# Performance work log

Measured on AMD Instinct MI355X. Metric: run time of the kernel, lower is better.

## Reference

```python
import jax, jax.numpy as jnp
import numpy as np
from jax import lax

IMG_DIM = 512
D_MODEL = 768
N_LAYER = 12
D_INNER = 2 * D_MODEL          # 1536
D_STATE = 16
D_CONV = 4
DT_RANK = (D_MODEL + 15) // 16 # 48
BATCH = 4
SEQ = 256


def setup_inputs() -> dict:
    key = jax.random.key(0)
    ks = jax.random.split(key, 16)
    s = 0.02
    inp = {
        "frames_rep": jax.random.normal(ks[0], (BATCH, SEQ, IMG_DIM), jnp.float32),
        "fproj_w": jax.random.normal(ks[1], (IMG_DIM, D_MODEL), jnp.float32) * s,
        "fproj_b": jnp.zeros((D_MODEL,), jnp.float32),
        "norm_w": jnp.ones((N_LAYER, D_MODEL), jnp.float32),
        "in_w": jax.random.normal(ks[2], (N_LAYER, D_MODEL, 2 * D_INNER), jnp.float32) * s,
        "conv_w": jax.random.normal(ks[3], (N_LAYER, D_INNER, D_CONV), jnp.float32) * s,
        "conv_b": jnp.zeros((N_LAYER, D_INNER), jnp.float32),
        "xproj_w": jax.random.normal(ks[4], (N_LAYER, D_INNER, DT_RANK + 2 * D_STATE), jnp.float32) * s,
        "dt_w": jax.random.normal(ks[5], (N_LAYER, DT_RANK, D_INNER), jnp.float32) * s,
        "dt_b": jnp.full((N_LAYER, D_INNER), -2.0, jnp.float32),  # softplus(-2)~0.13
        "A_log": jnp.broadcast_to(jnp.log(jnp.arange(1, D_STATE + 1, dtype=jnp.float32)), (N_LAYER, D_INNER, D_STATE)) * jnp.ones((N_LAYER, D_INNER, 1)),
        "D_param": jnp.ones((N_LAYER, D_INNER), jnp.float32),
        "out_w": jax.random.normal(ks[6], (N_LAYER, D_INNER, D_MODEL), jnp.float32) * s,
        "normf_w": jnp.ones((D_MODEL,), jnp.float32),
    }
    return inp


def _rmsnorm(x, w, eps=1e-5):
    return x * lax.rsqrt(jnp.mean(x * x, axis=-1, keepdims=True) + eps) * w


def _mamba_layer(x, in_w, conv_w, conv_b, xproj_w, dt_w, dt_b, A_log, D_param, out_w):
    # x: (B, L, D_MODEL)
    B, L, _ = x.shape
    xz = x @ in_w                                  # (B, L, 2*di)
    xi, res = jnp.split(xz, 2, axis=-1)            # each (B, L, di)
    # depthwise causal conv over time
    xc = jnp.transpose(xi, (0, 2, 1))              # (B, di, L)
    xc = lax.conv_general_dilated(
        xc, conv_w[:, None, :], (1,), [(D_CONV - 1, 0)],
        feature_group_count=D_INNER)
    xi = jax.nn.silu(jnp.transpose(xc + conv_b[None, :, None], (0, 2, 1)))
    # input-dependent SSM parameters
    x_dbl = xi @ xproj_w                           # (B, L, dt_rank + 2n)
    delta = x_dbl[..., :DT_RANK]
    Bm = x_dbl[..., DT_RANK:DT_RANK + D_STATE]     # (B, L, n)
    Cm = x_dbl[..., DT_RANK + D_STATE:]            # (B, L, n)
    delta = jax.nn.softplus(delta @ dt_w + dt_b)   # (B, L, di)
    A = -jnp.exp(A_log)                            # (di, n)
    deltaA = jnp.exp(delta[..., None] * A)                               # (B, L, di, n)
    deltaBu = delta[..., None] * Bm[:, :, None, :] * xi[..., None]       # (B, L, di, n)

    def step(h, inp):
        dA, dBu, c = inp
        h = dA * h + dBu                           # (B, di, n)
        y = jnp.einsum('bdn,bn->bd', h, c)
        return h, y

    xs = (deltaA.transpose(1, 0, 2, 3), deltaBu.transpose(1, 0, 2, 3), Cm.transpose(1, 0, 2))
    h0 = jnp.zeros((B, D_INNER, D_STATE), x.dtype)
    _, ys = lax.scan(step, h0, xs)                 # (L, B, di)
    y = ys.transpose(1, 0, 2) + xi * D_param
    y = y * jax.nn.silu(res)
    return y @ out_w                               # (B, L, D_MODEL)


def reference(frames_rep, fproj_w, fproj_b, norm_w, in_w, conv_w, conv_b,
              xproj_w, dt_w, dt_b, A_log, D_param, out_w, normf_w):
    h = jax.nn.relu(frames_rep @ fproj_w + fproj_b)       # (B, L, D_MODEL)
    for i in range(N_LAYER):
        h = h + _mamba_layer(_rmsnorm(h, norm_w[i]), in_w[i], conv_w[i], conv_b[i],
                             xproj_w[i], dt_w[i], dt_b[i], A_log[i], D_param[i], out_w[i])
    return _rmsnorm(h, normf_w)
```

## Files before the change

### kernel.cpp

```cpp
#include <hip/hip_runtime.h>
#include <hip/hip_bf16.h>
#include <cmath>

#define IMG_DIM 512
#define D_MODEL 768
#define N_LAYER 12
#define D_INNER 1536
#define D_STATE 16
#define D_CONV 4
#define DT_RANK 48
#define BATCH 4
#define SEQ 256
#define M_TOK (BATCH * SEQ)
#define XPROJ_N (DT_RANK + 2 * D_STATE)
#define KSPLIT 16
#define NCHUNK 16
#define CLEN 16
#define LOG2E 1.4426950408889634f

typedef __attribute__((ext_vector_type(8))) short bf16x8;
typedef __attribute__((ext_vector_type(8))) unsigned short u16x8;
typedef __attribute__((ext_vector_type(4))) float f32x4;
typedef __hip_bfloat16 bf16;

__device__ __forceinline__ float softplus_f(float v) {
    return v > 20.f ? v : log1pf(expf(v));
}
__device__ __forceinline__ float b2f(bf16 v) { return __bfloat162float(v); }
__device__ __forceinline__ float us2f(unsigned short v) {
    return __uint_as_float(((unsigned)v) << 16);
}

__device__ __forceinline__ void gl_lds16(const char* g, char* l) {
    __builtin_amdgcn_global_load_lds(
        (const __attribute__((address_space(1))) unsigned int*)g,
        (__attribute__((address_space(3))) unsigned int*)l,
        16, 0, 0);
}

__global__ __launch_bounds__(256) void wcvt_t_k(
    const float* __restrict__ W, bf16* __restrict__ WT, int K, int N)
{
    __shared__ float tile[32][33];
    W  += (size_t)blockIdx.z * K * N;
    WT += (size_t)blockIdx.z * K * N;
    const int tx = threadIdx.x & 31;
    const int ty4 = (threadIdx.x >> 5) * 4;
    const int n0 = blockIdx.x * 32, k0 = blockIdx.y * 32;
    #pragma unroll
    for (int r = 0; r < 4; ++r)
        tile[ty4 + r][tx] = (n0 + tx < N)
            ? W[(size_t)(k0 + ty4 + r) * N + n0 + tx] : 0.f;
    __syncthreads();
    #pragma unroll
    for (int r = 0; r < 4; ++r)
        if (n0 + ty4 + r < N)
            WT[(size_t)(n0 + ty4 + r) * K + k0 + tx] =
                __float2bfloat16(tile[tx][ty4 + r]);
}

__global__ __launch_bounds__(256) void cvt_bf16_k(
    const float* __restrict__ in, bf16* __restrict__ out, int n)
{
    int i = blockIdx.x * 256 + threadIdx.x;
    if (i < n) out[i] = __float2bfloat16(in[i]);
}

__global__ __launch_bounds__(256) void dtw_cvt_k(
    const float* __restrict__ dt_w, bf16* __restrict__ dtwT)
{
    int idx = blockIdx.x * 256 + threadIdx.x;
    int k = idx & 63;
    int n = (idx >> 6) % D_INNER;
    int l = idx / (64 * D_INNER);
    dtwT[idx] = (k < DT_RANK)
        ? __float2bfloat16(dt_w[((size_t)l * DT_RANK + k) * D_INNER + n])
        : bf16(0.f);
}

__global__ __launch_bounds__(256) void a2_k(
    const float* __restrict__ A_log, float* __restrict__ A2)
{
    int idx = blockIdx.x * 256 + threadIdx.x;
    A2[idx] = -expf(A_log[idx]) * LOG2E;
}

template <int EPI, typename OT>
__global__ __launch_bounds__(256) void gemm_bf16(
    const bf16* __restrict__ A,
    const bf16* __restrict__ BT,
    OT* __restrict__ C, int ldc, int K,
    const float* __restrict__ bias)
{
    __shared__ __align__(16) char lds[2][16384];
    const int tid = threadIdx.x;
    const int lane = tid & 63;
    const int wid = tid >> 6;
    const int wr = wid >> 1, wc = wid & 1;
    const size_t rowBase = blockIdx.x * 64;
    const size_t colBase = blockIdx.y * 64;

    const int r0 = tid >> 3;
    const int cb0 = (tid & 7) * 16;
    const int slot = tid * 16;
    const size_t gOffSw = (size_t)r0 * K * 2 + (cb0 ^ ((r0 & 7) << 4));
    const size_t aStep = (size_t)32 * K * 2;
    const char* gA = (const char*)(A + rowBase * K);
    const char* gB = (const char*)(BT + colBase * K);

    const int lrow = lane & 15;
    const int kg = (lane >> 4) * 16;
    const int swz = (lane & 7) << 4;

    f32x4 acc[2][2] = {};
    const int nt = K >> 6;

    {
        char* L = &lds[0][0];
        gl_lds16(gA + gOffSw,          L + slot);
        gl_lds16(gA + gOffSw + aStep,  L + 4096 + slot);
        gl_lds16(gB + gOffSw,          L + 8192 + slot);
        gl_lds16(gB + gOffSw + aStep,  L + 12288 + slot);
    }
    __syncthreads();

    for (int t = 0; t < nt; ++t) {
        const int cur = t & 1;
        if (t + 1 < nt) {
            char* L = &lds[cur ^ 1][0];
            size_t go = gOffSw + (size_t)(t + 1) * 128;
            gl_lds16(gA + go,          L + slot);
            gl_lds16(gA + go + aStep,  L + 4096 + slot);
            gl_lds16(gB + go,          L + 8192 + slot);
            gl_lds16(gB + go + aStep,  L + 12288 + slot);
        }
        #pragma unroll
        for (int kk = 0; kk < 2; ++kk) {
            const int col = (kk * 64 + kg) ^ swz;
            bf16x8 a0 = *(const bf16x8*)(&lds[cur][(wr * 32 +      lrow) * 128 + col]);
            bf16x8 a1 = *(const bf16x8*)(&lds[cur][(wr * 32 + 16 + lrow) * 128 + col]);
            bf16x8 b0 = *(const bf16x8*)(&lds[cur][8192 + (wc * 32 +      lrow) * 128 + col]);
            bf16x8 b1 = *(const bf16x8*)(&lds[cur][8192 + (wc * 32 + 16 + lrow) * 128 + col]);
            acc[0][0] = __builtin_amdgcn_mfma_f32_16x16x32_bf16(a0, b0, acc[0][0], 0, 0, 0);
            acc[0][1] = __builtin_amdgcn_mfma_f32_16x16x32_bf16(a0, b1, acc[0][1], 0, 0, 0);
            acc[1][0] = __builtin_amdgcn_mfma_f32_16x16x32_bf16(a1, b0, acc[1][0], 0, 0, 0);
            acc[1][1] = __builtin_amdgcn_mfma_f32_16x16x32_bf16(a1, b1, acc[1][1], 0, 0, 0);
        }
        __syncthreads();
    }

    const int mBase = (int)rowBase + wr * 32 + (lane >> 4) * 4;
    const int nBase = (int)colBase + wc * 32 + (lane & 15);
    #pragma unroll
    for (int i = 0; i < 2; ++i)
        #pragma unroll
        for (int j = 0; j < 2; ++j)
            #pragma unroll
            for (int rg = 0; rg < 4; ++rg) {
                int cc = nBase + j * 16;
                size_t idx = (size_t)(mBase + i * 16 + rg) * ldc + cc;
                float v = acc[i][j][rg];
                if (EPI == 0) {
                    C[idx] = (OT)v;
                } else if (EPI == 1) {
                    v += bias[cc];
                    C[idx] = (OT)(v > 0.f ? v : 0.f);
                } else if (EPI == 2) {
                    v += bias[cc];
                    C[idx] = (OT)softplus_f(v);
                } else {
                    C[idx] += v;
                }
            }
}

__global__ __launch_bounds__(256) void xproj_gemm_k(
    const bf16* __restrict__ xc_bf,
    const bf16* __restrict__ xprojT,
    float* __restrict__ part)
{
    const int lane = threadIdx.x & 63;
    const int w = threadIdx.x >> 6;
    const int m0 = blockIdx.x * 64 + w * 16;
    const int ks = blockIdx.y;
    const int KS = D_INNER / KSPLIT;
    const int k0 = ks * KS;

    const int arow = m0 + (lane & 15);
    const int kgrp = (lane >> 4) * 8;

    f32x4 acc[5] = {};
    const bf16* ap = xc_bf + (size_t)arow * D_INNER + kgrp;
    const bf16* bp = xprojT + (size_t)(lane & 15) * D_INNER + kgrp;

    for (int k = k0; k < k0 + KS; k += 32) {
        bf16x8 a = *(const bf16x8*)(ap + k);
        #pragma unroll
        for (int f = 0; f < 5; ++f) {
            bf16x8 b = *(const bf16x8*)(bp + (size_t)f * 16 * D_INNER + k);
            acc[f] = __builtin_amdgcn_mfma_f32_16x16x32_bf16(a, b, acc[f], 0, 0, 0);
        }
    }

    float* out = part + (size_t)ks * M_TOK * XPROJ_N;
    const int rowb = blockIdx.x * 64 + w * 16 + (lane >> 4) * 4;
    #pragma unroll
    for (int f = 0; f < 5; ++f)
        #pragma unroll
        for (int rg = 0; rg < 4; ++rg)
            out[(size_t)(rowb + rg) * XPROJ_N + f * 16 + (lane & 15)] = acc[f][rg];
}

__global__ __launch_bounds__(256) void xproj_reduce_k(
    const float* __restrict__ part, float* __restrict__ xdbl,
    bf16* __restrict__ dtin)
{
    int idx = blockIdx.x * 256 + threadIdx.x;
    float s = 0.f;
    #pragma unroll
    for (int p = 0; p < KSPLIT; ++p)
        s += part[(size_t)p * M_TOK * XPROJ_N + idx];
    xdbl[idx] = s;
    int col = idx % XPROJ_N;
    int row = idx / XPROJ_N;
    if (col < DT_RANK)
        dtin[(size_t)row * 64 + col] = __float2bfloat16(s);
    else if (col >= 64)
        dtin[(size_t)row * 64 + col - 16] = bf16(0.f);
}

template <typename OT>
__global__ __launch_bounds__(256) void rmsnorm_k(
    const float* __restrict__ x, const float* __restrict__ w,
    OT* __restrict__ o)
{
    const int row = blockIdx.x;
    const float* xr = x + (size_t)row * D_MODEL;
    float v[3];
    float s = 0.f;
    #pragma unroll
    for (int i = 0; i < 3; ++i) {
        v[i] = xr[threadIdx.x + i * 256];
        s = fmaf(v[i], v[i], s);
    }
    #pragma unroll
    for (int off = 32; off > 0; off >>= 1) s += __shfl_down(s, off);
    __shared__ float red[4];
    if ((threadIdx.x & 63) == 0) red[threadIdx.x >> 6] = s;
    __syncthreads();
    float tot = red[0] + red[1] + red[2] + red[3];
    float r = rsqrtf(tot * (1.f / D_MODEL) + 1e-5f);
    OT* orow = o + (size_t)row * D_MODEL;
    #pragma unroll
    for (int i = 0; i < 3; ++i) {
        int c = threadIdx.x + i * 256;
        orow[c] = (OT)(v[i] * r * w[c]);
    }
}

__global__ __launch_bounds__(256) void conv_silu_k(
    const bf16* __restrict__ xz, const float* __restrict__ cw,
    const float* __restrict__ cb, bf16* __restrict__ xc_bf)
{
    int v = blockIdx.x * 256 + threadIdx.x;
    int d8 = (v * 8) % D_INNER;
    int bt = (v * 8) / D_INNER;
    int t = bt & (SEQ - 1);
    int b = bt >> 8;

    float acc[8];
    {
        const float4* cbp = (const float4*)(cb + d8);
        float4 c0 = cbp[0], c1 = cbp[1];
        acc[0] = c0.x; acc[1] = c0.y; acc[2] = c0.z; acc[3] = c0.w;
        acc[4] = c1.x; acc[5] = c1.y; acc[6] = c1.z; acc[7] = c1.w;
    }
    float4 wv[8];
    #pragma unroll
    for (int j = 0; j < 8; ++j)
        wv[j] = *(const float4*)(cw + (size_t)(d8 + j) * 4);

    #pragma unroll
    for (int k = 0; k < 4; ++k) {
        int tt = t - 3 + k;
        if (tt >= 0) {
            u16x8 xv = *(const u16x8*)(xz + (size_t)(b * SEQ + tt) * (2 * D_INNER) + d8);
            #pragma unroll
            for (int j = 0; j < 8; ++j) {
                float wk = (k == 0) ? wv[j].x : (k == 1) ? wv[j].y
                         : (k == 2) ? wv[j].z : wv[j].w;
                acc[j] = fmaf(us2f(xv[j]), wk, acc[j]);
            }
        }
    }

    __align__(16) bf16 ob[8];
    #pragma unroll
    for (int j = 0; j < 8; ++j) {
        float a = acc[j];
        float s = a / (1.f + expf(-a));
        ob[j] = __float2bfloat16(s);
    }
    *(uint4*)(xc_bf + (size_t)v * 8) = *(const uint4*)ob;
}

__global__ __launch_bounds__(256) void scan_part_k(
    const bf16* __restrict__ delta,
    const bf16* __restrict__ xc,
    const float* __restrict__ xdbl,
    const float* __restrict__ A2,
    const float* __restrict__ D_param,
    float* __restrict__ cumdv,
    float* __restrict__ ypart,
    float* __restrict__ hpart)
{
    __shared__ float sBC[CLEN][32];
    const int tid = threadIdx.x;
    const int dgrp  = blockIdx.x % 6;
    const int chunk = (blockIdx.x / 6) & (NCHUNK - 1);
    const int b     = blockIdx.x / (6 * NCHUNK);
    const int d  = dgrp * 256 + tid;
    const int t0 = chunk * CLEN;

    {
        int r = tid >> 5, c = tid & 31;
        sBC[r][c]     = xdbl[(size_t)(b * SEQ + t0 + r) * XPROJ_N + DT_RANK + c];
        sBC[r + 8][c] = xdbl[(size_t)(b * SEQ + t0 + r + 8) * XPROJ_N + DT_RANK + c];
    }

    float a2[16];
    {
        const float4* ap = (const float4*)(A2 + (size_t)d * 16);
        #pragma unroll
        for (int q = 0; q < 4; ++q) {
            float4 vv = ap[q];
            a2[q * 4 + 0] = vv.x; a2[q * 4 + 1] = vv.y;
            a2[q * 4 + 2] = vv.z; a2[q * 4 + 3] = vv.w;
        }
    }
    const float Dp = D_param[d];

    const size_t base = (size_t)(b * SEQ + t0) * D_INNER + d;
    const bf16* dp = delta + base;
    const bf16* up = xc + base;

    float dvv[CLEN], uvv[CLEN];
    #pragma unroll
    for (int s = 0; s < CLEN; ++s) {
        dvv[s] = b2f(dp[(size_t)s * D_INNER]);
        uvv[s] = b2f(up[(size_t)s * D_INNER]);
    }
    __syncthreads();

    float h[16];
    #pragma unroll
    for (int n = 0; n < 16; ++n) h[n] = 0.f;
    float cum = 0.f;

    #pragma unroll
    for (int s = 0; s < CLEN; ++s) {
        float dv = dvv[s], u = uvv[s];
        cum += dv;
        cumdv[base + (size_t)s * D_INNER] = cum;
        float du = dv * u;
        float yv = 0.f;
        #pragma unroll
        for (int n = 0; n < 16; ++n) {
            float dA = exp2f(dv * a2[n]);
            h[n] = fmaf(dA, h[n], du * sBC[s][n]);
            yv = fmaf(h[n], sBC[s][16 + n], yv);
        }
        ypart[base + (size_t)s * D_INNER] = fmaf(u, Dp, yv);
    }

    float4* hp = (float4*)(hpart + (((size_t)b * NCHUNK + chunk) * D_INNER + d) * 16);
    #pragma unroll
    for (int q = 0; q < 4; ++q) {
        float4 vv;
        vv.x = h[q * 4 + 0]; vv.y = h[q * 4 + 1];
        vv.z = h[q * 4 + 2]; vv.w = h[q * 4 + 3];
        hp[q] = vv;
    }
}

__global__ __launch_bounds__(256) void scan_pref_k(
    const float* __restrict__ cumdv,
    const float* __restrict__ hpart,
    const float* __restrict__ A2,
    float* __restrict__ hinb)
{
    int idx = blockIdx.x * 256 + threadIdx.x;
    int n = idx & 15;
    int r = idx >> 4;
    int d = r % D_INNER;
    int b = r / D_INNER;
    float a2 = A2[(size_t)d * 16 + n];
    float hin = 0.f;
    #pragma unroll
    for (int c = 0; c < NCHUNK; ++c) {
        hinb[(((size_t)b * NCHUNK + c) * D_INNER + d) * 16 + n] = hin;
        float sdv = cumdv[(size_t)(b * SEQ + c * CLEN + CLEN - 1) * D_INNER + d];
        float hp  = hpart[(((size_t)b * NCHUNK + c) * D_INNER + d) * 16 + n];
        hin = fmaf(hin, exp2f(a2 * sdv), hp);
    }
}

__global__ __launch_bounds__(256) void scan_fix_k(
    const float* __restrict__ ypart,
    const float* __restrict__ cumdv,
    const float* __restrict__ xdbl,
    const bf16* __restrict__ xz,
    const float* __restrict__ A2,
    const float* __restrict__ hinb,
    bf16* __restrict__ y)
{
    __shared__ float sC[16];
    int idx = blockIdx.x * 256 + threadIdx.x;
    int d = idx % D_INNER;
    int bt = idx / D_INNER;
    int t = bt & (SEQ - 1);
    int b = bt >> 8;
    int chunk = t >> 4;

    if (threadIdx.x < 16)
        sC[threadIdx.x] = xdbl[(size_t)bt * XPROJ_N + DT_RANK + D_STATE + threadIdx.x];
    __syncthreads();

    float cum = cumdv[idx];
    float yp  = ypart[idx];
    float res = b2f(xz[(size_t)bt * 2 * D_INNER + D_INNER + d]);

    const float4* hp = (const float4*)(hinb + (((size_t)b * NCHUNK + chunk) * D_INNER + d) * 16);
    const float4* ap = (const float4*)(A2 + (size_t)d * 16);

    float corr = 0.f;
    #pragma unroll
    for (int q = 0; q < 4; ++q) {
        float4 hv = hp[q];
        float4 av = ap[q];
        corr = fmaf(exp2f(av.x * cum) * hv.x, sC[q * 4 + 0], corr);
        corr = fmaf(exp2f(av.y * cum) * hv.y, sC[q * 4 + 1], corr);
        corr = fmaf(exp2f(av.z * cum) * hv.z, sC[q * 4 + 2], corr);
        corr = fmaf(exp2f(av.w * cum) * hv.w, sC[q * 4 + 3], corr);
    }
    float sr = res / (1.f + expf(-res));
    y[idx] = __float2bfloat16((yp + corr) * sr);
}

extern "C" void kernel_launch(void* const* d_in, const int* in_sizes, int n_in,
                              void* d_out, int out_size, void* d_ws, size_t ws_size,
                              hipStream_t stream)
{
    const float* frames  = (const float*)d_in[0];
    const float* fproj_w = (const float*)d_in[1];
    const float* fproj_b = (const float*)d_in[2];
    const float* norm_w  = (const float*)d_in[3];
    const float* in_w    = (const float*)d_in[4];
    const float* conv_w  = (const float*)d_in[5];
    const float* conv_b  = (const float*)d_in[6];
    const float* xproj_w = (const float*)d_in[7];
    const float* dt_w    = (const float*)d_in[8];
    const float* dt_b    = (const float*)d_in[9];
    const float* A_log   = (const float*)d_in[10];
    const float* D_param = (const float*)d_in[11];
    const float* out_w   = (const float*)d_in[12];
    const float* normf_w = (const float*)d_in[13];

    char* ws = (char*)d_ws;
    float* h      = (float*)ws;        ws += (size_t)M_TOK * D_MODEL * 4;
    float* xdbl   = (float*)ws;        ws += (size_t)M_TOK * XPROJ_N * 4;
    float* part   = (float*)ws;        ws += (size_t)KSPLIT * M_TOK * XPROJ_N * 4;
    float* cumdv  = (float*)ws;        ws += (size_t)M_TOK * D_INNER * 4;
    float* ypartb = (float*)ws;        ws += (size_t)M_TOK * D_INNER * 4;
    float* hpartb = (float*)ws;        ws += (size_t)BATCH * NCHUNK * D_INNER * 16 * 4;
    float* hinb   = (float*)ws;        ws += (size_t)BATCH * NCHUNK * D_INNER * 16 * 4;
    float* A2all  = (float*)ws;        ws += (size_t)N_LAYER * D_INNER * 16 * 4;
    bf16* xz_bf   = (bf16*)ws;         ws += (size_t)M_TOK * 2 * D_INNER * 2;
    bf16* xc_bf   = (bf16*)ws;         ws += (size_t)M_TOK * D_INNER * 2;
    bf16* delta_bf= (bf16*)ws;         ws += (size_t)M_TOK * D_INNER * 2;
    bf16* x_bf    = (bf16*)ws;         ws += (size_t)M_TOK * D_MODEL * 2;
    bf16* y_bf    = (bf16*)ws;         ws += (size_t)M_TOK * D_INNER * 2;
    bf16* dtin    = (bf16*)ws;         ws += (size_t)M_TOK * 64 * 2;
    bf16* fr_bf   = (bf16*)ws;         ws += (size_t)M_TOK * IMG_DIM * 2;
    bf16* fp_wT   = (bf16*)ws;         ws += (size_t)D_MODEL * IMG_DIM * 2;
    bf16* in_wT   = (bf16*)ws;         ws += (size_t)N_LAYER * 2 * D_INNER * D_MODEL * 2;
    bf16* out_wT  = (bf16*)ws;         ws += (size_t)N_LAYER * D_MODEL * D_INNER * 2;
    bf16* xprojT  = (bf16*)ws;         ws += (size_t)N_LAYER * XPROJ_N * D_INNER * 2;
    bf16* dt_wT   = (bf16*)ws;         ws += (size_t)N_LAYER * D_INNER * 64 * 2;

    dim3 blk(256);

    cvt_bf16_k<<<(M_TOK * IMG_DIM) / 256, blk, 0, stream>>>(
        frames, fr_bf, M_TOK * IMG_DIM);
    wcvt_t_k<<<dim3(D_MODEL / 32, IMG_DIM / 32, 1), blk, 0, stream>>>(
        fproj_w, fp_wT, IMG_DIM, D_MODEL);
    wcvt_t_k<<<dim3(2 * D_INNER / 32, D_MODEL / 32, N_LAYER), blk, 0, stream>>>(
        in_w, in_wT, D_MODEL, 2 * D_INNER);
    wcvt_t_k<<<dim3(D_MODEL / 32, D_INNER / 32, N_LAYER), blk, 0, stream>>>(
        out_w, out_wT, D_INNER, D_MODEL);
    wcvt_t_k<<<dim3((XPROJ_N + 31) / 32, D_INNER / 32, N_LAYER), blk, 0, stream>>>(
        xproj_w, xprojT, D_INNER, XPROJ_N);
    dtw_cvt_k<<<(N_LAYER * D_INNER * 64) / 256, blk, 0, stream>>>(dt_w, dt_wT);
    a2_k<<<(N_LAYER * D_INNER * 16) / 256, blk, 0, stream>>>(A_log, A2all);

    gemm_bf16<1, float><<<dim3(M_TOK / 64, D_MODEL / 64), blk, 0, stream>>>(
        fr_bf, fp_wT, h, D_MODEL, IMG_DIM, fproj_b);

    for (int i = 0; i < N_LAYER; ++i) {
        const bf16* in_wTi   = in_wT  + (size_t)i * 2 * D_INNER * D_MODEL;
        const bf16* out_wTi  = out_wT + (size_t)i * D_MODEL * D_INNER;
        const bf16* xprojTi  = xprojT + (size_t)i * XPROJ_N * D_INNER;
        const bf16* dt_wTi   = dt_wT  + (size_t)i * D_INNER * 64;
        const float* A2i     = A2all  + (size_t)i * D_INNER * 16;
        const float* conv_wi = conv_w + (size_t)i * D_INNER * D_CONV;
        const float* conv_bi = conv_b + (size_t)i * D_INNER;
        const float* dt_bi   = dt_b   + (size_t)i * D_INNER;
        const float* D_parami= D_param+ (size_t)i * D_INNER;
        const float* norm_wi = norm_w + (size_t)i * D_MODEL;

        rmsnorm_k<bf16><<<M_TOK, blk, 0, stream>>>(h, norm_wi, x_bf);
        gemm_bf16<0, bf16><<<dim3(M_TOK / 64, (2 * D_INNER) / 64), blk, 0, stream>>>(
            x_bf, in_wTi, xz_bf, 2 * D_INNER, D_MODEL, nullptr);
        conv_silu_k<<<(M_TOK * D_INNER / 8) / 256, blk, 0, stream>>>(
            xz_bf, conv_wi, conv_bi, xc_bf);
        xproj_gemm_k<<<dim3(M_TOK / 64, KSPLIT), blk, 0, stream>>>(
            xc_bf, xprojTi, part);
        xproj_reduce_k<<<(M_TOK * XPROJ_N) / 256, blk, 0, stream>>>(
            part, xdbl, dtin);
        gemm_bf16<2, bf16><<<dim3(M_TOK / 64, D_INNER / 64), blk, 0, stream>>>(
            dtin, dt_wTi, delta_bf, D_INNER, 64, dt_bi);
        scan_part_k<<<BATCH * NCHUNK * (D_INNER / 256), blk, 0, stream>>>(
            delta_bf, xc_bf, xdbl, A2i, D_parami, cumdv, ypartb, hpartb);
        scan_pref_k<<<(BATCH * D_INNER * 16) / 256, blk, 0, stream>>>(
            cumdv, hpartb, A2i, hinb);
        scan_fix_k<<<(M_TOK * D_INNER) / 256, blk, 0, stream>>>(
            ypartb, cumdv, xdbl, xz_bf, A2i, hinb, y_bf);
        gemm_bf16<3, float><<<dim3(M_TOK / 64, D_MODEL / 64), blk, 0, stream>>>(
            y_bf, out_wTi, h, D_MODEL, D_INNER, nullptr);
    }

    rmsnorm_k<float><<<M_TOK, blk, 0, stream>>>(h, normf_w, (float*)d_out);
}
```

Measured before the change: 1.282 ms.

## Restructure chunked scan to recompute chunk pass with carried-in state

The chunked selective scan changes from part/prefix/fix, which wrote per-token cumulative deltas and partial outputs, to part/prefix/final. The first pass now stores only per-chunk state and delta sums. The final pass reruns the chunk recurrence starting from the prefix state and fuses the D skip term and the SiLU gate. This removes two full-size fp32 intermediate arrays and their global traffic, at the cost of running the 16-state exp/FMA recurrence twice per token.

```diff
diff --git a/kernel.cpp b/kernel.cpp
--- a/kernel.cpp
+++ b/kernel.cpp
@@ -309,10 +309,104 @@
     const bf16* __restrict__ xc,
     const float* __restrict__ xdbl,
     const float* __restrict__ A2,
+    float* __restrict__ dvsum,
+    float* __restrict__ hpart)
+{
+    __shared__ float sB[CLEN][16];
+    const int tid = threadIdx.x;
+    const int dgrp  = blockIdx.x % 6;
+    const int chunk = (blockIdx.x / 6) & (NCHUNK - 1);
+    const int b     = blockIdx.x / (6 * NCHUNK);
+    const int d  = dgrp * 256 + tid;
+    const int t0 = chunk * CLEN;
+
+    if (tid < CLEN * 16) {
+        int r = tid >> 4, c = tid & 15;
+        sB[r][c] = xdbl[(size_t)(b * SEQ + t0 + r) * XPROJ_N + DT_RANK + c];
+    }
+
+    float a2[16];
+    {
+        const float4* ap = (const float4*)(A2 + (size_t)d * 16);
+        #pragma unroll
+        for (int q = 0; q < 4; ++q) {
+            float4 vv = ap[q];
+            a2[q * 4 + 0] = vv.x; a2[q * 4 + 1] = vv.y;
+            a2[q * 4 + 2] = vv.z; a2[q * 4 + 3] = vv.w;
+        }
+    }
+
+    const size_t base = (size_t)(b * SEQ + t0) * D_INNER + d;
+    const bf16* dp = delta + base;
+    const bf16* up = xc + base;
+
+    float dvv[CLEN], uvv[CLEN];
+    #pragma unroll
+    for (int s = 0; s < CLEN; ++s) {
+        dvv[s] = b2f(dp[(size_t)s * D_INNER]);
+        uvv[s] = b2f(up[(size_t)s * D_INNER]);
+    }
+    __syncthreads();
+
+    float h[16];
+    #pragma unroll
+    for (int n = 0; n < 16; ++n) h[n] = 0.f;
+    float cum = 0.f;
+
+    #pragma unroll
+    for (int s = 0; s < CLEN; ++s) {
+        float dv = dvv[s];
+        cum += dv;
+        float du = dv * uvv[s];
+        #pragma unroll
+        for (int n = 0; n < 16; ++n) {
+            float dA = exp2f(dv * a2[n]);
+            h[n] = fmaf(dA, h[n], du * sB[s][n]);
+        }
+    }
+
+    dvsum[((size_t)b * NCHUNK + chunk) * D_INNER + d] = cum;
+    float4* hp = (float4*)(hpart + (((size_t)b * NCHUNK + chunk) * D_INNER + d) * 16);
+    #pragma unroll
+    for (int q = 0; q < 4; ++q) {
+        float4 vv;
+        vv.x = h[q * 4 + 0]; vv.y = h[q * 4 + 1];
+        vv.z = h[q * 4 + 2]; vv.w = h[q * 4 + 3];
+        hp[q] = vv;
+    }
+}
+
+__global__ __launch_bounds__(256) void scan_pref_k(
+    const float* __restrict__ dvsum,
+    const float* __restrict__ hpart,
+    const float* __restrict__ A2,
+    float* __restrict__ hinb)
+{
+    int idx = blockIdx.x * 256 + threadIdx.x;
+    int n = idx & 15;
+    int r = idx >> 4;
+    int d = r % D_INNER;
+    int b = r / D_INNER;
+    float a2 = A2[(size_t)d * 16 + n];
+    float hin = 0.f;
+    #pragma unroll
+    for (int c = 0; c < NCHUNK; ++c) {
+        hinb[(((size_t)b * NCHUNK + c) * D_INNER + d) * 16 + n] = hin;
+        float sdv = dvsum[((size_t)b * NCHUNK + c) * D_INNER + d];
+        float hp  = hpart[(((size_t)b * NCHUNK + c) * D_INNER + d) * 16 + n];
+        hin = fmaf(hin, exp2f(a2 * sdv), hp);
+    }
+}
+
+__global__ __launch_bounds__(256) void scan_fin_k(
+    const bf16* __restrict__ delta,
+    const bf16* __restrict__ xc,
+    const float* __restrict__ xdbl,
+    const bf16* __restrict__ xz,
+    const float* __restrict__ A2,
     const float* __restrict__ D_param,
-    float* __restrict__ cumdv,
-    float* __restrict__ ypart,
-    float* __restrict__ hpart)
+    const float* __restrict__ hinb,
+    bf16* __restrict__ y)
 {
     __shared__ float sBC[CLEN][32];
     const int tid = threadIdx.x;
@@ -343,6 +437,8 @@
     const size_t base = (size_t)(b * SEQ + t0) * D_INNER + d;
     const bf16* dp = delta + base;
     const bf16* up = xc + base;
+    const bf16* rp = xz + (size_t)(b * SEQ + t0) * 2 * D_INNER + D_INNER + d;
+    bf16* yp = y + base;
 
     float dvv[CLEN], uvv[CLEN];
     #pragma unroll
@@ -350,18 +446,22 @@
         dvv[s] = b2f(dp[(size_t)s * D_INNER]);
         uvv[s] = b2f(up[(size_t)s * D_INNER]);
     }
+
+    float h[16];
+    {
+        const float4* hp = (const float4*)(hinb + (((size_t)b * NCHUNK + chunk) * D_INNER + d) * 16);
+        #pragma unroll
+        for (int q = 0; q < 4; ++q) {
+            float4 vv = hp[q];
+            h[q * 4 + 0] = vv.x; h[q * 4 + 1] = vv.y;
+            h[q * 4 + 2] = vv.z; h[q * 4 + 3] = vv.w;
+        }
+    }
     __syncthreads();
-
-    float h[16];
-    #pragma unroll
-    for (int n = 0; n < 16; ++n) h[n] = 0.f;
-    float cum = 0.f;
 
     #pragma unroll
     for (int s = 0; s < CLEN; ++s) {
         float dv = dvv[s], u = uvv[s];
-        cum += dv;
-        cumdv[base + (size_t)s * D_INNER] = cum;
         float du = dv * u;
         float yv = 0.f;
         #pragma unroll
@@ -370,81 +470,11 @@
             h[n] = fmaf(dA, h[n], du * sBC[s][n]);
             yv = fmaf(h[n], sBC[s][16 + n], yv);
         }
-        ypart[base + (size_t)s * D_INNER] = fmaf(u, Dp, yv);
-    }
-
-    float4* hp = (float4*)(hpart + (((size_t)b * NCHUNK + chunk) * D_INNER + d) * 16);
-    #pragma unroll
-    for (int q = 0; q < 4; ++q) {
-        float4 vv;
-        vv.x = h[q * 4 + 0]; vv.y = h[q * 4 + 1];
-        vv.z = h[q * 4 + 2]; vv.w = h[q * 4 + 3];
-        hp[q] = vv;
-    }
-}
-
-__global__ __launch_bounds__(256) void scan_pref_k(
-    const float* __restrict__ cumdv,
-    const float* __restrict__ hpart,
-    const float* __restrict__ A2,
-    float* __restrict__ hinb)
-{
-    int idx = blockIdx.x * 256 + threadIdx.x;
-    int n = idx & 15;
-    int r = idx >> 4;
-    int d = r % D_INNER;
-    int b = r / D_INNER;
-    float a2 = A2[(size_t)d * 16 + n];
-    float hin = 0.f;
-    #pragma unroll
-    for (int c = 0; c < NCHUNK; ++c) {
-        hinb[(((size_t)b * NCHUNK + c) * D_INNER + d) * 16 + n] = hin;
-        float sdv = cumdv[(size_t)(b * SEQ + c * CLEN + CLEN - 1) * D_INNER + d];
-        float hp  = hpart[(((size_t)b * NCHUNK + c) * D_INNER + d) * 16 + n];
-        hin = fmaf(hin, exp2f(a2 * sdv), hp);
-    }
-}
-
-__global__ __launch_bounds__(256) void scan_fix_k(
-    const float* __restrict__ ypart,
-    const float* __restrict__ cumdv,
-    const float* __restrict__ xdbl,
-    const bf16* __restrict__ xz,
-    const float* __restrict__ A2,
-    const float* __restrict__ hinb,
-    bf16* __restrict__ y)
-{
-    __shared__ float sC[16];
-    int idx = blockIdx.x * 256 + threadIdx.x;
-    int d = idx % D_INNER;
-    int bt = idx / D_INNER;
-    int t = bt & (SEQ - 1);
-    int b = bt >> 8;
-    int chunk = t >> 4;
-
-    if (threadIdx.x < 16)
-        sC[threadIdx.x] = xdbl[(size_t)bt * XPROJ_N + DT_RANK + D_STATE + threadIdx.x];
-    __syncthreads();
-
-    float cum = cumdv[idx];
-    float yp  = ypart[idx];
-    float res = b2f(xz[(size_t)bt * 2 * D_INNER + D_INNER + d]);
-
-    const float4* hp = (const float4*)(hinb + (((size_t)b * NCHUNK + chunk) * D_INNER + d) * 16);
-    const float4* ap = (const float4*)(A2 + (size_t)d * 16);
-
-    float corr = 0.f;
-    #pragma unroll
-    for (int q = 0; q < 4; ++q) {
-        float4 hv = hp[q];
-        float4 av = ap[q];
-        corr = fmaf(exp2f(av.x * cum) * hv.x, sC[q * 4 + 0], corr);
-        corr = fmaf(exp2f(av.y * cum) * hv.y, sC[q * 4 + 1], corr);
-        corr = fmaf(exp2f(av.z * cum) * hv.z, sC[q * 4 + 2], corr);
-        corr = fmaf(exp2f(av.w * cum) * hv.w, sC[q * 4 + 3], corr);
-    }
-    float sr = res / (1.f + expf(-res));
-    y[idx] = __float2bfloat16((yp + corr) * sr);
+        float res = b2f(rp[(size_t)s * 2 * D_INNER]);
+        float sr = res / (1.f + expf(-res));
+        yp[(size_t)s * D_INNER] =
+            __float2bfloat16(fmaf(u, Dp, yv) * sr);
+    }
 }
 
 extern "C" void kernel_launch(void* const* d_in, const int* in_sizes, int n_in,
@@ -470,8 +500,7 @@
     float* h      = (float*)ws;        ws += (size_t)M_TOK * D_MODEL * 4;
     float* xdbl   = (float*)ws;        ws += (size_t)M_TOK * XPROJ_N * 4;
     float* part   = (float*)ws;        ws += (size_t)KSPLIT * M_TOK * XPROJ_N * 4;
-    float* cumdv  = (float*)ws;        ws += (size_t)M_TOK * D_INNER * 4;
-    float* ypartb = (float*)ws;        ws += (size_t)M_TOK * D_INNER * 4;
+    float* dvsum  = (float*)ws;        ws += (size_t)BATCH * NCHUNK * D_INNER * 4;
     float* hpartb = (float*)ws;        ws += (size_t)BATCH * NCHUNK * D_INNER * 16 * 4;
     float* hinb   = (float*)ws;        ws += (size_t)BATCH * NCHUNK * D_INNER * 16 * 4;
     float* A2all  = (float*)ws;        ws += (size_t)N_LAYER * D_INNER * 16 * 4;
@@ -530,11 +559,11 @@
         gemm_bf16<2, bf16><<<dim3(M_TOK / 64, D_INNER / 64), blk, 0, stream>>>(
             dtin, dt_wTi, delta_bf, D_INNER, 64, dt_bi);
         scan_part_k<<<BATCH * NCHUNK * (D_INNER / 256), blk, 0, stream>>>(
-            delta_bf, xc_bf, xdbl, A2i, D_parami, cumdv, ypartb, hpartb);
+            delta_bf, xc_bf, xdbl, A2i, dvsum, hpartb);
         scan_pref_k<<<(BATCH * D_INNER * 16) / 256, blk, 0, stream>>>(
-            cumdv, hpartb, A2i, hinb);
-        scan_fix_k<<<(M_TOK * D_INNER) / 256, blk, 0, stream>>>(
-            ypartb, cumdv, xdbl, xz_bf, A2i, hinb, y_bf);
+            dvsum, hpartb, A2i, hinb);
+        scan_fin_k<<<BATCH * NCHUNK * (D_INNER / 256), blk, 0, stream>>>(
+            delta_bf, xc_bf, xdbl, xz_bf, A2i, D_parami, hinb, y_bf);
         gemm_bf16<3, float><<<dim3(M_TOK / 64, D_MODEL / 64), blk, 0, stream>>>(
             y_bf, out_wTi, h, D_MODEL, D_INNER, nullptr);
     }
```

New measurement: 1.166 ms (median of 2 runs). 1.1x faster.
